# Kernel optimization log

Hardware: AMD Instinct MI355X
Metric: run time of the kernel (lower is better)

Reference implementation:

```python
import jax, jax.numpy as jnp
import numpy as np
from jax import lax

B, T, V, C = 16, 128, 137, 3
IOC = [(64, 64), (64, 128), (128, 256)]  # (in_c, out_c), all strides 1
OUT0 = 64
K = 9
PAD = (K - 1) // 2
NUM_CLASS = 226
DELTA = 0.5
BN_EPS = 1e-5


def setup_inputs() -> dict:
    key = jax.random.key(0)
    ks = jax.random.split(key, 16)
    inp = {"X": jax.random.normal(ks[0], (B, T, V, C), dtype=jnp.float32)}
    # data_bn params over V*C channels
    inp["bn_gamma"] = jnp.ones((V * C,), jnp.float32)
    inp["bn_beta"] = jnp.zeros((V * C,), jnp.float32)
    # gtcn0 conv
    inp["w0"] = jax.random.normal(ks[1], (OUT0, C, K, 1), jnp.float32) * np.sqrt(2.0 / (C * K))
    inp["b0"] = jnp.zeros((OUT0,), jnp.float32)
    for i, (ic, oc) in enumerate(IOC):
        inp[f"w{i+1}"] = jax.random.normal(ks[2 + i], (oc, ic, K, 1), jnp.float32) * np.sqrt(2.0 / (ic * K))
        inp[f"b{i+1}"] = jnp.zeros((oc,), jnp.float32)
    inp["fc_w"] = jax.random.normal(ks[8], (NUM_CLASS, IOC[-1][1]), jnp.float32) * 0.02
    inp["fc_b"] = jnp.zeros((NUM_CLASS,), jnp.float32)
    return inp


def _adj(X):
    # Gaussian-kernel affinity per (batch, frame): exp(-||xi-xj|| / (2*delta^2)).
    # Original builds this on CPU with scipy.cdist inside torch.tensor (detached),
    # so we stop gradients through it.
    Xs = lax.stop_gradient(X)  # [B,T,V,C]
    diff = Xs[:, :, :, None, :] - Xs[:, :, None, :, :]  # [B,T,V,V,C]
    dist = jnp.sqrt(jnp.sum(diff * diff, axis=-1))       # euclidean, like cdist
    return jnp.exp(-dist / (2.0 * DELTA ** 2))            # [B,T,V,V]


def _conv(x, w, b):
    # Conv2d kernel (K,1), padding ((K-1)//2, 0), stride (1,1)
    y = lax.conv_general_dilated(x, w, window_strides=(1, 1),
                                 padding=[(PAD, PAD), (0, 0)],
                                 dimension_numbers=("NCHW", "OIHW", "NCHW"))
    return y + b[None, :, None, None]


def reference(X, bn_gamma, bn_beta, w0, b0, w1, b1, w2, b2, w3, b3, fc_w, fc_b):
    A = _adj(X)  # [B,T,V,V]
    # data_bn: BatchNorm1d over V*C channels (training-mode batch stats)
    Xr = jnp.einsum("btvc->bvct", X).reshape(B, V * C, T)
    mean = Xr.mean(axis=(0, 2), keepdims=True)
    var = Xr.var(axis=(0, 2), keepdims=True)
    Xn = (Xr - mean) * jax.lax.rsqrt(var + BN_EPS)
    Xn = Xn * bn_gamma[None, :, None] + bn_beta[None, :, None]
    x = jnp.einsum("bvct->bctv", Xn.reshape(B, V, C, T))  # [B,C,T,V]
    x = _conv(x, w0, b0)
    for w, b in ((w1, b1), (w2, b2), (w3, b3)):
        ax = jnp.einsum("bctv,btvw->bctw", x, A)  # graph matmul X @ A per (b,t)
        x = jax.nn.relu(_conv(ax, w, b))
    x = x.mean(axis=(2, 3))  # [B, C_out]
    return x @ fc_w.T + fc_b  # [B, num_class]
```

## Files before the change

kernel.cpp:

```cpp
#include <hip/hip_runtime.h>
#include <hip/hip_bf16.h>
#include <math.h>

#define BB 16
#define TT 128
#define VV 137
#define CCH 3
#define NN (VV*TT)
#define NCLS 226
#define APITCH 23040

typedef __attribute__((ext_vector_type(8))) short bf16x8;
typedef __attribute__((ext_vector_type(4))) float f32x4;

__device__ __forceinline__ unsigned short f2bf(float x) {
  __hip_bfloat16 h = __float2bfloat16(x);
  return *reinterpret_cast<unsigned short*>(&h);
}

__device__ __forceinline__ void gld_lds16(const unsigned short* src, unsigned short* ldst) {
  __builtin_amdgcn_global_load_lds(
      (const __attribute__((address_space(1))) void*)src,
      (__attribute__((address_space(3))) void*)ldst, 16, 0, 0);
}

__global__ void bn_stats_kernel(const float* __restrict__ X,
                                const float* __restrict__ gamma,
                                const float* __restrict__ beta,
                                float* __restrict__ scale,
                                float* __restrict__ shift) {
  const int ch = blockIdx.x;
  const int v = ch / CCH, c = ch % CCH;
  const int tid = threadIdx.x;
  float s = 0.f, q = 0.f;
  for (int idx = tid; idx < BB*TT; idx += 256) {
    float x = X[(idx*VV + v)*CCH + c];
    s += x; q += x*x;
  }
  #pragma unroll
  for (int off = 32; off > 0; off >>= 1) {
    s += __shfl_down(s, off, 64);
    q += __shfl_down(q, off, 64);
  }
  __shared__ float ls[4], lq[4];
  const int wid = tid >> 6, lane = tid & 63;
  if (lane == 0) { ls[wid] = s; lq[wid] = q; }
  __syncthreads();
  if (tid == 0) {
    float S = ls[0]+ls[1]+ls[2]+ls[3];
    float Q = lq[0]+lq[1]+lq[2]+lq[3];
    const float inv_n = 1.f / (BB*TT);
    float mean = S * inv_n;
    float var = Q * inv_n - mean*mean;
    float sc = gamma[ch] * rsqrtf(var + 1e-5f);
    scale[ch] = sc;
    shift[ch] = beta[ch] - mean * sc;
  }
}

__global__ void bn_apply_v(const float* __restrict__ X,
                           const float* __restrict__ scale,
                           const float* __restrict__ shift,
                           unsigned short* __restrict__ xn) {
  const int o = blockIdx.x*256 + threadIdx.x;
  if (o >= BB*NN*CCH) return;
  const int c = o % CCH;
  const int n = (o / CCH) % NN;
  const int b = o / (CCH*NN);
  const int v = n >> 7, t = n & 127;
  const int ch = v*CCH + c;
  float val = X[((b*TT + t)*VV + v)*CCH + c] * scale[ch] + shift[ch];
  xn[o] = f2bf(val);
}

__global__ void wtrans_kernel(const float* __restrict__ w, unsigned short* __restrict__ wT,
                              int OC, int IC) {
  const int o = blockIdx.x*256 + threadIdx.x;
  if (o >= OC*IC*9) return;
  const int ic = o % IC;
  const int oc = (o / IC) % OC;
  const int kk = o / (IC*OC);
  wT[o] = f2bf(w[(oc*IC + ic)*9 + kk]);
}

__global__ void w0trans_kernel(const float* __restrict__ w0, unsigned short* __restrict__ w0T) {
  const int o = blockIdx.x*256 + threadIdx.x;
  if (o >= 64*32) return;
  const int k = o % 32, oc = o / 32;
  const int kk = k / 3, ic = k % 3;
  w0T[o] = (k < 27) ? f2bf(w0[(oc*3 + ic)*9 + kk]) : (unsigned short)0;
}

__global__ void zero_kernel(float* __restrict__ p, int n) {
  const int i = blockIdx.x*256 + threadIdx.x;
  if (i < n) p[i] = 0.f;
}

__global__ __launch_bounds__(256)
void adj_v(const float* __restrict__ X, unsigned short* __restrict__ A) {
  __shared__ float Xs[3][144];
  const int b = blockIdx.x / TT, t = blockIdx.x % TT;
  const int tid = threadIdx.x;
  for (int i = tid; i < 3*VV; i += 256) {
    const int c = i / VV, v = i % VV;
    Xs[c][v] = X[((b*TT + t)*VV + v)*CCH + c];
  }
  __syncthreads();
  unsigned short* Ab = A + (size_t)blockIdx.x * APITCH;
  for (int e = tid; e < 144*160; e += 256) {
    const int w = e / 160, v = e % 160;
    unsigned short val = 0;
    if (w < VV && v < VV) {
      const float d0 = Xs[0][v]-Xs[0][w];
      const float d1 = Xs[1][v]-Xs[1][w];
      const float d2 = Xs[2][v]-Xs[2][w];
      val = f2bf(__expf(-2.f * sqrtf(d0*d0 + d1*d1 + d2*d2)));
    }
    Ab[e] = val;
  }
}

__global__ __launch_bounds__(256)
void conv0_v(const unsigned short* __restrict__ xn,
             const unsigned short* __restrict__ w0T,
             const float* __restrict__ bias,
             unsigned short* __restrict__ outp) {
  __shared__ unsigned short im_s[128*40];
  __shared__ unsigned short w_s[64*40];
  __shared__ unsigned short ob[128*72];
  const int tid = threadIdx.x;
  const int v0 = blockIdx.x % 137;
  const int b  = blockIdx.x / 137;
  const int wave = tid >> 6, lane = tid & 63, quad = lane >> 4, l15 = lane & 15;
  const int mh = wave * 32;

  {
    const int row = tid >> 2, cg = tid & 3;
    *(uint4*)&w_s[row*40 + cg*8] = *(const uint4*)(w0T + row*32 + cg*8);
  }
  for (int e = tid; e < 128*32; e += 256) {
    const int t = e >> 5, k = e & 31;
    unsigned short val = 0;
    if (k < 27) {
      const int kk = k / 3, ic = k % 3;
      const int tp = t + kk - 4;
      if (tp >= 0 && tp < TT)
        val = xn[((size_t)b*NN + (size_t)v0*TT + tp)*3 + ic];
    }
    im_s[t*40 + k] = val;
  }
  __syncthreads();

  f32x4 acc[2][4];
  #pragma unroll
  for (int mt = 0; mt < 2; ++mt)
    #pragma unroll
    for (int ct = 0; ct < 4; ++ct) acc[mt][ct] = (f32x4){0.f,0.f,0.f,0.f};

  bf16x8 af[2], bfr[4];
  #pragma unroll
  for (int mt = 0; mt < 2; ++mt)
    af[mt] = *(const bf16x8*)&im_s[(mh + mt*16 + l15)*40 + quad*8];
  #pragma unroll
  for (int ct = 0; ct < 4; ++ct)
    bfr[ct] = *(const bf16x8*)&w_s[(ct*16 + l15)*40 + quad*8];
  #pragma unroll
  for (int mt = 0; mt < 2; ++mt)
    #pragma unroll
    for (int ct = 0; ct < 4; ++ct)
      acc[mt][ct] = __builtin_amdgcn_mfma_f32_16x16x32_bf16(af[mt], bfr[ct], acc[mt][ct], 0, 0, 0);

  #pragma unroll
  for (int mt = 0; mt < 2; ++mt) {
    const int tb = mh + mt*16 + quad*4;
    #pragma unroll
    for (int ct = 0; ct < 4; ++ct) {
      const int oc = ct*16 + l15;
      const float bv = bias[oc];
      #pragma unroll
      for (int r = 0; r < 4; ++r)
        ob[(tb + r)*72 + oc] = f2bf(acc[mt][ct][r] + bv);
    }
  }
  __syncthreads();
  for (int rr = 0; rr < 4; ++rr) {
    const int idx = rr*256 + tid;
    const int t = idx >> 3, cg = idx & 7;
    uint4 val = *(const uint4*)&ob[t*72 + cg*8];
    *(uint4*)(outp + ((size_t)b*NN + (size_t)v0*TT + t)*64 + cg*8) = val;
  }
}

template<int IC, int OCB, int VROWS, int WDBUF, int RELU, int FUSE>
__global__ __launch_bounds__(256)
void conv_v3(const unsigned short* __restrict__ in,
             const unsigned short* __restrict__ wT,
             const float* __restrict__ bias,
             unsigned short* __restrict__ outp,
             float* __restrict__ mout,
             const unsigned short* __restrict__ zbuf,
             int OCtot, int nocb) {
  constexpr int NCT  = (VROWS == 2) ? OCB/16 : OCB/32;
  constexpr int NWIN = 136*IC/512;
  constexpr int TWIN = VROWS*NWIN;
  constexpr int WWIN = OCB*IC/512;
  constexpr int GPR  = IC/8;
  constexpr int RPW  = 512/IC;
  constexpr int INSZ = VROWS*136*IC;
  constexpr int WSZ  = OCB*IC;
  constexpr int NWB  = WDBUF ? 2 : 1;
  constexpr int OCP  = OCB + 8;
  constexpr int OBSZ = FUSE ? 0 : VROWS*128*OCP;
  constexpr int TOT  = (INSZ + NWB*WSZ > OBSZ) ? (INSZ + NWB*WSZ) : OBSZ;
  __shared__ unsigned short sh[TOT];
  unsigned short* in_s = sh;
  unsigned short* ob = sh;

  const int tid = threadIdx.x;
  const int wave = tid >> 6, lane = tid & 63, quad = lane >> 4, l15 = lane & 15;
  const int nv = (VROWS == 2) ? 69 : 137;
  const int grp  = blockIdx.x % nv;
  const int ocby = (blockIdx.x / nv) % nocb;
  const int b    = blockIdx.x / (nv*nocb);
  const int v0 = grp * VROWS;
  const int ocb0 = ocby * OCB;
  const int vr  = (VROWS == 2) ? (wave >> 1) : 0;
  const int mhl = (VROWS == 2) ? ((wave & 1) * 64) : ((wave >> 1) * 64);
  const int chb = (VROWS == 2) ? 0 : ((wave & 1) * (OCB >> 1));
  const bool vok = (VROWS == 1) || ((v0 + vr) < VV);

  const int lrow = lane / GPR;
  const int lg   = lane % GPR;

  #pragma unroll
  for (int wi = 0; wi < (TWIN+3)/4; ++wi) {
    const int W = wave + 4*wi;
    if (W < TWIN) {
      const int vrW = W / NWIN;
      const int rl = (W % NWIN)*RPW + lrow;
      const int t = rl - 4;
      const int sg = lg ^ (rl & 7);
      const unsigned short* src = (t >= 0 && t < TT && (v0+vrW) < VV)
          ? in + ((size_t)b*NN + (size_t)(v0+vrW)*TT + t)*IC + (sg<<3)
          : zbuf + lane*8;
      gld_lds16(src, in_s + W*512);
    }
  }
  auto stage_w = [&](int kk, int buf) {
    unsigned short* wb = sh + INSZ + buf*WSZ;
    #pragma unroll
    for (int wi = 0; wi < WWIN/4; ++wi) {
      const int W = wave + 4*wi;
      const int row = W*RPW + lrow;
      const int sg = lg ^ (row & 7);
      gld_lds16(wT + ((size_t)kk*OCtot + ocb0 + row)*IC + (sg<<3), wb + W*512);
    }
  };

  f32x4 acc[4][NCT];
  #pragma unroll
  for (int mt = 0; mt < 4; ++mt)
    #pragma unroll
    for (int ct = 0; ct < NCT; ++ct) acc[mt][ct] = (f32x4){0.f,0.f,0.f,0.f};

  auto compute_kk = [&](int kk, int buf) {
    const unsigned short* wb = sh + INSZ + buf*WSZ;
    #pragma unroll
    for (int ks = 0; ks < IC/32; ++ks) {
      const int G = ks*4 + quad;
      bf16x8 af[4], bfr[NCT];
      #pragma unroll
      for (int mt = 0; mt < 4; ++mt) {
        const int row = mhl + mt*16 + l15 + kk;
        af[mt] = *(const bf16x8*)&in_s[vr*(136*IC) + row*IC + ((G ^ (row & 7)) << 3)];
      }
      #pragma unroll
      for (int ct = 0; ct < NCT; ++ct) {
        const int row = chb + ct*16 + l15;
        bfr[ct] = *(const bf16x8*)&wb[row*IC + ((G ^ (row & 7)) << 3)];
      }
      #pragma unroll
      for (int mt = 0; mt < 4; ++mt)
        #pragma unroll
        for (int ct = 0; ct < NCT; ++ct)
          acc[mt][ct] = __builtin_amdgcn_mfma_f32_16x16x32_bf16(af[mt], bfr[ct], acc[mt][ct], 0, 0, 0);
    }
  };

  if (WDBUF) {
    stage_w(0, 0);
    __syncthreads();
    for (int kk = 0; kk < 9; ++kk) {
      if (kk < 8) stage_w(kk+1, (kk+1) & 1);
      compute_kk(kk, kk & 1);
      __syncthreads();
    }
  } else {
    for (int kk = 0; kk < 9; ++kk) {
      stage_w(kk, 0);
      __syncthreads();
      compute_kk(kk, 0);
      __syncthreads();
    }
  }

  if (FUSE) {
    if (vok) {
      #pragma unroll
      for (int ct = 0; ct < NCT; ++ct) {
        const int oc = ocb0 + chb + ct*16 + l15;
        const float bv = bias[oc];
        float s = 0.f;
        #pragma unroll
        for (int mt = 0; mt < 4; ++mt)
          #pragma unroll
          for (int r = 0; r < 4; ++r) {
            float x = acc[mt][ct][r] + bv;
            if (RELU) x = fmaxf(x, 0.f);
            s += x;
          }
        s += __shfl_down(s, 32, 64);
        s += __shfl_down(s, 16, 64);
        if (lane < 16) atomicAdd(&mout[(size_t)b*OCtot + oc], s * (1.f / NN));
      }
    }
  } else {
    #pragma unroll
    for (int mt = 0; mt < 4; ++mt) {
      const int ro = vr*128 + mhl + mt*16 + quad*4;
      #pragma unroll
      for (int ct = 0; ct < NCT; ++ct) {
        const int oc = chb + ct*16 + l15;
        const float bv = bias[ocb0 + oc];
        #pragma unroll
        for (int r = 0; r < 4; ++r) {
          float x = acc[mt][ct][r] + bv;
          if (RELU) x = fmaxf(x, 0.f);
          ob[(ro + r)*OCP + oc] = f2bf(x);
        }
      }
    }
    __syncthreads();
    constexpr int GPO = OCB/8;
    #pragma unroll
    for (int it = 0; it < VROWS*128*GPO/256; ++it) {
      const int task = it*256 + tid;
      const int ro = task / GPO, g = task % GPO;
      const int vrow = v0 + (ro >> 7);
      if (vrow < VV) {
        uint4 val = *(const uint4*)&ob[ro*OCP + g*8];
        *(uint4*)(outp + ((size_t)b*NN + (size_t)vrow*TT + (ro & 127))*OCB + g*8) = val;
      }
    }
  }
}

__global__ __launch_bounds__(256)
void gmm_v3(const unsigned short* __restrict__ A,
            const unsigned short* __restrict__ act,
            unsigned short* __restrict__ outp,
            int Cfull) {
  __shared__ unsigned short sh[12288 + APITCH];
  unsigned short* xt = sh;
  unsigned short* As = sh + 12288;
  unsigned short* ob = sh + 12288;
  const int bt = blockIdx.x;
  const int b = bt / TT, t = bt % TT;
  const int ch = blockIdx.y;
  const int tid = threadIdx.x;
  const int wave = tid >> 6, lane = tid & 63, quad = lane >> 4, l15 = lane & 15;

  const unsigned short* Abt = A + (size_t)bt * APITCH;
  for (int W = wave; W < 45; W += 4)
    gld_lds16(Abt + W*512 + lane*8, As + W*512);

  #pragma unroll
  for (int it = 0; it < 5; ++it) {
    const int task = it*256 + tid;
    const int v = task >> 3, g = task & 7;
    uint4 val = {0u,0u,0u,0u};
    if (v < VV)
      val = *(const uint4*)(act + ((size_t)b*NN + (size_t)v*TT + t)*Cfull + ch*64 + g*8);
    const unsigned short* pv = (const unsigned short*)&val;
    const int vg = v >> 3, vrm = v & 7;
    #pragma unroll
    for (int j = 0; j < 8; ++j) {
      const int c = g*8 + j;
      const int slot = ((vg ^ (c & 7) ^ ((c >> 3) & 7)) << 3) | vrm;
      xt[c*192 + slot] = pv[j];
    }
  }
  __syncthreads();

  f32x4 acc[9];
  #pragma unroll
  for (int ct = 0; ct < 9; ++ct) acc[ct] = (f32x4){0.f,0.f,0.f,0.f};

  const int m = wave*16 + l15;
  #pragma unroll
  for (int ks = 0; ks < 5; ++ks) {
    const int G = ks*4 + quad;
    const int slot = (G ^ (m & 7) ^ ((m >> 3) & 7)) << 3;
    const bf16x8 af = *(const bf16x8*)&xt[m*192 + slot];
    #pragma unroll
    for (int ct = 0; ct < 9; ++ct) {
      const bf16x8 bfv = *(const bf16x8*)&As[(ct*16 + l15)*160 + ks*32 + quad*8];
      acc[ct] = __builtin_amdgcn_mfma_f32_16x16x32_bf16(af, bfv, acc[ct], 0, 0, 0);
    }
  }
  __syncthreads();

  #pragma unroll
  for (int ct = 0; ct < 9; ++ct) {
    const int w = ct*16 + l15;
    #pragma unroll
    for (int r = 0; r < 4; ++r) {
      const int c = wave*16 + quad*4 + r;
      ob[w*72 + c] = f2bf(acc[ct][r]);
    }
  }
  __syncthreads();
  {
    const int wl = tid >> 3, cg = tid & 7;
    #pragma unroll
    for (int rr = 0; rr < 5; ++rr) {
      const int w = rr*32 + wl;
      if (w < VV) {
        uint4 val = *(const uint4*)&ob[w*72 + cg*8];
        *(uint4*)(outp + ((size_t)b*NN + (size_t)w*TT + t)*Cfull + ch*64 + cg*8) = val;
      }
    }
  }
}

__global__ void fc_kernel(const float* __restrict__ mean,
                          const float* __restrict__ fcw,
                          const float* __restrict__ fcb,
                          float* __restrict__ out) {
  const int b = blockIdx.x;
  __shared__ float ms[256];
  const int tid = threadIdx.x;
  ms[tid] = mean[b*256 + tid];
  __syncthreads();
  if (tid < NCLS) {
    float acc = fcb[tid];
    for (int c = 0; c < 256; ++c) acc = fmaf(ms[c], fcw[tid*256 + c], acc);
    out[b*NCLS + tid] = acc;
  }
}

extern "C" void kernel_launch(void* const* d_in, const int* in_sizes, int n_in,
                              void* d_out, int out_size, void* d_ws, size_t ws_size,
                              hipStream_t stream) {
  const float* X    = (const float*)d_in[0];
  const float* bn_g = (const float*)d_in[1];
  const float* bn_b = (const float*)d_in[2];
  const float* w0   = (const float*)d_in[3];
  const float* cb0  = (const float*)d_in[4];
  const float* w1   = (const float*)d_in[5];
  const float* cb1  = (const float*)d_in[6];
  const float* w2   = (const float*)d_in[7];
  const float* cb2  = (const float*)d_in[8];
  const float* w3   = (const float*)d_in[9];
  const float* cb3  = (const float*)d_in[10];
  const float* fcw  = (const float*)d_in[11];
  const float* fcb  = (const float*)d_in[12];
  float* out = (float*)d_out;

  unsigned char* W = (unsigned char*)d_ws;
  size_t off = 0;
  auto alloc = [&](size_t bytes) -> void* {
    void* p = W + off;
    off += (bytes + 255) & ~(size_t)255;
    return p;
  };
  float* meanb  = (float*)alloc(BB*256*4);
  float* zbuf_f = (float*)alloc(2048);
  float* scale  = (float*)alloc(512*4);
  float* shiftb = (float*)alloc(512*4);
  unsigned short* w0T = (unsigned short*)alloc(64*32*2);
  unsigned short* wT1 = (unsigned short*)alloc((size_t)9*64*64*2);
  unsigned short* wT2 = (unsigned short*)alloc((size_t)9*128*64*2);
  unsigned short* wT3 = (unsigned short*)alloc((size_t)9*256*128*2);
  unsigned short* xn  = (unsigned short*)alloc((size_t)BB*NN*3*2);
  const size_t fixedB = off;
  const size_t perB = 2*((size_t)NN*128*2 + 256) + ((size_t)TT*APITCH*2 + 256);

  int g = 1;
  if (ws_size > fixedB + perB) {
    size_t gg = (ws_size - fixedB) / perB;
    g = (gg >= BB) ? BB : (int)gg;
  }
  unsigned short* P  = (unsigned short*)alloc((size_t)g*NN*128*2);
  unsigned short* Q  = (unsigned short*)alloc((size_t)g*NN*128*2);
  unsigned short* Ab = (unsigned short*)alloc((size_t)g*TT*APITCH*2);
  const unsigned short* zbuf = (const unsigned short*)zbuf_f;

  bn_stats_kernel<<<411, 256, 0, stream>>>(X, bn_g, bn_b, scale, shiftb);
  bn_apply_v<<<(BB*NN*3 + 255)/256, 256, 0, stream>>>(X, scale, shiftb, xn);
  w0trans_kernel<<<(64*32 + 255)/256, 256, 0, stream>>>(w0, w0T);
  wtrans_kernel<<<(9*64*64   + 255)/256, 256, 0, stream>>>(w1, wT1, 64, 64);
  wtrans_kernel<<<(9*128*64  + 255)/256, 256, 0, stream>>>(w2, wT2, 128, 64);
  wtrans_kernel<<<(9*256*128 + 255)/256, 256, 0, stream>>>(w3, wT3, 256, 128);
  zero_kernel<<<((BB*256 + 512) + 255)/256, 256, 0, stream>>>(meanb, BB*256 + 512);

  for (int b0 = 0; b0 < BB; b0 += g) {
    const int gb = (BB - b0 < g) ? (BB - b0) : g;
    const float* Xg = X + (size_t)b0 * TT * VV * CCH;
    const unsigned short* xng = xn + (size_t)b0 * NN * 3;
    float* mg = meanb + (size_t)b0 * 256;

    adj_v<<<gb*TT, 256, 0, stream>>>(Xg, Ab);
    conv0_v<<<137*gb, 256, 0, stream>>>(xng, w0T, cb0, P);
    gmm_v3<<<dim3(gb*TT, 1), 256, 0, stream>>>(Ab, P, Q, 64);
    conv_v3<64,64,1,1,1,0><<<137*gb, 256, 0, stream>>>(Q, wT1, cb1, P, nullptr, zbuf, 64, 1);
    gmm_v3<<<dim3(gb*TT, 1), 256, 0, stream>>>(Ab, P, Q, 64);
    conv_v3<64,128,1,1,1,0><<<137*gb, 256, 0, stream>>>(Q, wT2, cb2, P, nullptr, zbuf, 128, 1);
    gmm_v3<<<dim3(gb*TT, 2), 256, 0, stream>>>(Ab, P, Q, 128);
    conv_v3<128,128,1,0,1,1><<<137*2*gb, 256, 0, stream>>>(Q, wT3, cb3, nullptr, mg, zbuf, 256, 2);
  }

  fc_kernel<<<BB, 256, 0, stream>>>(meanb, fcw, fcb, out);
}
```

Before: 528.4 us.

## Load conv weights directly into registers with double-buffered prefetch, drop LDS weight staging

The temporal conv kernel no longer stages weight tiles in LDS with per-tap barriers. Each lane loads its MFMA B-fragments straight from global memory (L2-resident) into registers, ping-ponging two register buffers across k-steps, and the unused VROWS=2 path is removed. This cuts LDS size and the barriers inside the main loop, which may improve occupancy and overlap. In exchange every wave re-reads the weights from global or L2 and uses more registers, and load latency is only hidden by a one-step prefetch.

Measured after the change: 735.6 us. 39.2% more time.

```diff
diff --git a/kernel.cpp b/kernel.cpp
--- a/kernel.cpp
+++ b/kernel.cpp
@@ -191,70 +191,62 @@
   }
 }
 
-template<int IC, int OCB, int VROWS, int WDBUF, int RELU, int FUSE>
+template<int IC, int OCB, int RELU, int FUSE>
 __global__ __launch_bounds__(256)
-void conv_v3(const unsigned short* __restrict__ in,
+void conv_v4(const unsigned short* __restrict__ in,
              const unsigned short* __restrict__ wT,
              const float* __restrict__ bias,
              unsigned short* __restrict__ outp,
              float* __restrict__ mout,
              const unsigned short* __restrict__ zbuf,
              int OCtot, int nocb) {
-  constexpr int NCT  = (VROWS == 2) ? OCB/16 : OCB/32;
+  constexpr int NCT  = OCB/32;
+  constexpr int KS   = IC/32;
+  constexpr int NSTEP= 9*KS;
   constexpr int NWIN = 136*IC/512;
-  constexpr int TWIN = VROWS*NWIN;
-  constexpr int WWIN = OCB*IC/512;
   constexpr int GPR  = IC/8;
   constexpr int RPW  = 512/IC;
-  constexpr int INSZ = VROWS*136*IC;
-  constexpr int WSZ  = OCB*IC;
-  constexpr int NWB  = WDBUF ? 2 : 1;
+  constexpr int INSZ = 136*IC;
   constexpr int OCP  = OCB + 8;
-  constexpr int OBSZ = FUSE ? 0 : VROWS*128*OCP;
-  constexpr int TOT  = (INSZ + NWB*WSZ > OBSZ) ? (INSZ + NWB*WSZ) : OBSZ;
+  constexpr int OBSZ = FUSE ? 0 : 128*OCP;
+  constexpr int TOT  = (INSZ > OBSZ) ? INSZ : OBSZ;
   __shared__ unsigned short sh[TOT];
   unsigned short* in_s = sh;
   unsigned short* ob = sh;
 
   const int tid = threadIdx.x;
   const int wave = tid >> 6, lane = tid & 63, quad = lane >> 4, l15 = lane & 15;
-  const int nv = (VROWS == 2) ? 69 : 137;
-  const int grp  = blockIdx.x % nv;
-  const int ocby = (blockIdx.x / nv) % nocb;
-  const int b    = blockIdx.x / (nv*nocb);
-  const int v0 = grp * VROWS;
+  const int v0   = blockIdx.x % 137;
+  const int ocby = (blockIdx.x / 137) % nocb;
+  const int b    = blockIdx.x / (137*nocb);
   const int ocb0 = ocby * OCB;
-  const int vr  = (VROWS == 2) ? (wave >> 1) : 0;
-  const int mhl = (VROWS == 2) ? ((wave & 1) * 64) : ((wave >> 1) * 64);
-  const int chb = (VROWS == 2) ? 0 : ((wave & 1) * (OCB >> 1));
-  const bool vok = (VROWS == 1) || ((v0 + vr) < VV);
+  const int mhl = (wave >> 1) * 64;
+  const int chb = (wave & 1) * (OCB >> 1);
 
   const int lrow = lane / GPR;
   const int lg   = lane % GPR;
 
   #pragma unroll
-  for (int wi = 0; wi < (TWIN+3)/4; ++wi) {
+  for (int wi = 0; wi < (NWIN+3)/4; ++wi) {
     const int W = wave + 4*wi;
-    if (W < TWIN) {
-      const int vrW = W / NWIN;
-      const int rl = (W % NWIN)*RPW + lrow;
+    if (W < NWIN) {
+      const int rl = W*RPW + lrow;
       const int t = rl - 4;
       const int sg = lg ^ (rl & 7);
-      const unsigned short* src = (t >= 0 && t < TT && (v0+vrW) < VV)
-          ? in + ((size_t)b*NN + (size_t)(v0+vrW)*TT + t)*IC + (sg<<3)
+      const unsigned short* src = (t >= 0 && t < TT)
+          ? in + ((size_t)b*NN + (size_t)v0*TT + t)*IC + (sg<<3)
           : zbuf + lane*8;
       gld_lds16(src, in_s + W*512);
     }
   }
-  auto stage_w = [&](int kk, int buf) {
-    unsigned short* wb = sh + INSZ + buf*WSZ;
-    #pragma unroll
-    for (int wi = 0; wi < WWIN/4; ++wi) {
-      const int W = wave + 4*wi;
-      const int row = W*RPW + lrow;
-      const int sg = lg ^ (row & 7);
-      gld_lds16(wT + ((size_t)kk*OCtot + ocb0 + row)*IC + (sg<<3), wb + W*512);
-    }
+
+  const unsigned short* wbase = wT + ((size_t)(ocb0 + chb + l15))*IC + quad*8;
+  auto wload = [&](int s, bf16x8 (&wr)[NCT]) {
+    const int kk = s / KS, ks = s - kk*KS;
+    const unsigned short* p = wbase + ((size_t)kk*OCtot)*IC + ks*32;
+    #pragma unroll
+    for (int ct = 0; ct < NCT; ++ct)
+      wr[ct] = *(const bf16x8*)(p + ct*16*IC);
   };
 
   f32x4 acc[4][NCT];
@@ -263,71 +255,57 @@
     #pragma unroll
     for (int ct = 0; ct < NCT; ++ct) acc[mt][ct] = (f32x4){0.f,0.f,0.f,0.f};
 
-  auto compute_kk = [&](int kk, int buf) {
-    const unsigned short* wb = sh + INSZ + buf*WSZ;
-    #pragma unroll
-    for (int ks = 0; ks < IC/32; ++ks) {
-      const int G = ks*4 + quad;
-      bf16x8 af[4], bfr[NCT];
+  auto compute_step = [&](int kk, int ks, bf16x8 (&wr)[NCT]) {
+    const int G = ks*4 + quad;
+    bf16x8 af[4];
+    #pragma unroll
+    for (int mt = 0; mt < 4; ++mt) {
+      const int row = mhl + mt*16 + l15 + kk;
+      af[mt] = *(const bf16x8*)&in_s[row*IC + ((G ^ (row & 7)) << 3)];
+    }
+    #pragma unroll
+    for (int mt = 0; mt < 4; ++mt)
       #pragma unroll
-      for (int mt = 0; mt < 4; ++mt) {
-        const int row = mhl + mt*16 + l15 + kk;
-        af[mt] = *(const bf16x8*)&in_s[vr*(136*IC) + row*IC + ((G ^ (row & 7)) << 3)];
-      }
-      #pragma unroll
-      for (int ct = 0; ct < NCT; ++ct) {
-        const int row = chb + ct*16 + l15;
-        bfr[ct] = *(const bf16x8*)&wb[row*IC + ((G ^ (row & 7)) << 3)];
-      }
+      for (int ct = 0; ct < NCT; ++ct)
+        acc[mt][ct] = __builtin_amdgcn_mfma_f32_16x16x32_bf16(af[mt], wr[ct], acc[mt][ct], 0, 0, 0);
+  };
+
+  bf16x8 wA[NCT], wB[NCT];
+  wload(0, wA);
+  wload(1, wB);
+  __syncthreads();
+
+  #pragma unroll
+  for (int s = 0; s < NSTEP; s += 2) {
+    compute_step(s / KS, s % KS, wA);
+    if (s + 2 < NSTEP) wload(s + 2, wA);
+    compute_step((s+1) / KS, (s+1) % KS, wB);
+    if (s + 3 < NSTEP) wload(s + 3, wB);
+  }
+
+  if (FUSE) {
+    #pragma unroll
+    for (int ct = 0; ct < NCT; ++ct) {
+      const int oc = ocb0 + chb + ct*16 + l15;
+      const float bv = bias[oc];
+      float s = 0.f;
       #pragma unroll
       for (int mt = 0; mt < 4; ++mt)
         #pragma unroll
-        for (int ct = 0; ct < NCT; ++ct)
-          acc[mt][ct] = __builtin_amdgcn_mfma_f32_16x16x32_bf16(af[mt], bfr[ct], acc[mt][ct], 0, 0, 0);
-    }
-  };
-
-  if (WDBUF) {
-    stage_w(0, 0);
+        for (int r = 0; r < 4; ++r) {
+          float x = acc[mt][ct][r] + bv;
+          if (RELU) x = fmaxf(x, 0.f);
+          s += x;
+        }
+      s += __shfl_down(s, 32, 64);
+      s += __shfl_down(s, 16, 64);
+      if (lane < 16) atomicAdd(&mout[(size_t)b*OCtot + oc], s * (1.f / NN));
+    }
+  } else {
     __syncthreads();
-    for (int kk = 0; kk < 9; ++kk) {
-      if (kk < 8) stage_w(kk+1, (kk+1) & 1);
-      compute_kk(kk, kk & 1);
-      __syncthreads();
-    }
-  } else {
-    for (int kk = 0; kk < 9; ++kk) {
-      stage_w(kk, 0);
-      __syncthreads();
-      compute_kk(kk, 0);
-      __syncthreads();
-    }
-  }
-
-  if (FUSE) {
-    if (vok) {
-      #pragma unroll
-      for (int ct = 0; ct < NCT; ++ct) {
-        const int oc = ocb0 + chb + ct*16 + l15;
-        const float bv = bias[oc];
-        float s = 0.f;
-        #pragma unroll
-        for (int mt = 0; mt < 4; ++mt)
-          #pragma unroll
-          for (int r = 0; r < 4; ++r) {
-            float x = acc[mt][ct][r] + bv;
-            if (RELU) x = fmaxf(x, 0.f);
-            s += x;
-          }
-        s += __shfl_down(s, 32, 64);
-        s += __shfl_down(s, 16, 64);
-        if (lane < 16) atomicAdd(&mout[(size_t)b*OCtot + oc], s * (1.f / NN));
-      }
-    }
-  } else {
     #pragma unroll
     for (int mt = 0; mt < 4; ++mt) {
-      const int ro = vr*128 + mhl + mt*16 + quad*4;
+      const int ro = mhl + mt*16 + quad*4;
       #pragma unroll
       for (int ct = 0; ct < NCT; ++ct) {
         const int oc = chb + ct*16 + l15;
@@ -343,14 +321,11 @@
     __syncthreads();
     constexpr int GPO = OCB/8;
     #pragma unroll
-    for (int it = 0; it < VROWS*128*GPO/256; ++it) {
+    for (int it = 0; it < 128*GPO/256; ++it) {
       const int task = it*256 + tid;
       const int ro = task / GPO, g = task % GPO;
-      const int vrow = v0 + (ro >> 7);
-      if (vrow < VV) {
-        uint4 val = *(const uint4*)&ob[ro*OCP + g*8];
-        *(uint4*)(outp + ((size_t)b*NN + (size_t)vrow*TT + (ro & 127))*OCB + g*8) = val;
-      }
+      uint4 val = *(const uint4*)&ob[ro*OCP + g*8];
+      *(uint4*)(outp + ((size_t)b*NN + (size_t)v0*TT + ro)*OCB + g*8) = val;
     }
   }
 }
@@ -513,11 +488,11 @@
     adj_v<<<gb*TT, 256, 0, stream>>>(Xg, Ab);
     conv0_v<<<137*gb, 256, 0, stream>>>(xng, w0T, cb0, P);
     gmm_v3<<<dim3(gb*TT, 1), 256, 0, stream>>>(Ab, P, Q, 64);
-    conv_v3<64,64,1,1,1,0><<<137*gb, 256, 0, stream>>>(Q, wT1, cb1, P, nullptr, zbuf, 64, 1);
+    conv_v4<64,64,1,0><<<137*gb, 256, 0, stream>>>(Q, wT1, cb1, P, nullptr, zbuf, 64, 1);
     gmm_v3<<<dim3(gb*TT, 1), 256, 0, stream>>>(Ab, P, Q, 64);
-    conv_v3<64,128,1,1,1,0><<<137*gb, 256, 0, stream>>>(Q, wT2, cb2, P, nullptr, zbuf, 128, 1);
+    conv_v4<64,128,1,0><<<137*gb, 256, 0, stream>>>(Q, wT2, cb2, P, nullptr, zbuf, 128, 1);
     gmm_v3<<<dim3(gb*TT, 2), 256, 0, stream>>>(Ab, P, Q, 128);
-    conv_v3<128,128,1,0,1,1><<<137*2*gb, 256, 0, stream>>>(Q, wT3, cb3, nullptr, mg, zbuf, 256, 2);
+    conv_v4<128,128,1,1><<<137*2*gb, 256, 0, stream>>>(Q, wT3, cb3, nullptr, mg, zbuf, 256, 2);
   }
 
   fc_kernel<<<BB, 256, 0, stream>>>(meanb, fcw, fcb, out);
```

## Merge prep kernels into one launch and fuse BN apply into conv0

Applied to the files above, without the earlier changes.

Merges BN statistics, the first batch-group adjacency build, weight transposes and buffer zeroing into a single heterogeneous mega_prep kernel dispatched by block index. The separate BN-apply pass is removed: conv0 now reads raw X and applies scale/shift while building its im2col tile. This cuts several launches and one intermediate write/read of the normalized input. The cost is strided fp32 loads of X inside conv0 and a mixed-role prep kernel whose blocks have uneven work.

New measurement: 544.5 us. +3.0%, slower.

```diff
diff --git a/kernel.cpp b/kernel.cpp
--- a/kernel.cpp
+++ b/kernel.cpp
@@ -24,12 +24,12 @@
       (__attribute__((address_space(3))) void*)ldst, 16, 0, 0);
 }
 
-__global__ void bn_stats_kernel(const float* __restrict__ X,
-                                const float* __restrict__ gamma,
-                                const float* __restrict__ beta,
-                                float* __restrict__ scale,
-                                float* __restrict__ shift) {
-  const int ch = blockIdx.x;
+__device__ void bn_stats_body(const float* __restrict__ X,
+                              const float* __restrict__ gamma,
+                              const float* __restrict__ beta,
+                              float* __restrict__ scale,
+                              float* __restrict__ shift,
+                              int ch, float* sm) {
   const int v = ch / CCH, c = ch % CCH;
   const int tid = threadIdx.x;
   float s = 0.f, q = 0.f;
@@ -42,13 +42,12 @@
     s += __shfl_down(s, off, 64);
     q += __shfl_down(q, off, 64);
   }
-  __shared__ float ls[4], lq[4];
   const int wid = tid >> 6, lane = tid & 63;
-  if (lane == 0) { ls[wid] = s; lq[wid] = q; }
+  if (lane == 0) { sm[wid] = s; sm[4 + wid] = q; }
   __syncthreads();
   if (tid == 0) {
-    float S = ls[0]+ls[1]+ls[2]+ls[3];
-    float Q = lq[0]+lq[1]+lq[2]+lq[3];
+    float S = sm[0]+sm[1]+sm[2]+sm[3];
+    float Q = sm[4]+sm[5]+sm[6]+sm[7];
     const float inv_n = 1.f / (BB*TT);
     float mean = S * inv_n;
     float var = Q * inv_n - mean*mean;
@@ -58,62 +57,23 @@
   }
 }
 
-__global__ void bn_apply_v(const float* __restrict__ X,
-                           const float* __restrict__ scale,
-                           const float* __restrict__ shift,
-                           unsigned short* __restrict__ xn) {
-  const int o = blockIdx.x*256 + threadIdx.x;
-  if (o >= BB*NN*CCH) return;
-  const int c = o % CCH;
-  const int n = (o / CCH) % NN;
-  const int b = o / (CCH*NN);
-  const int v = n >> 7, t = n & 127;
-  const int ch = v*CCH + c;
-  float val = X[((b*TT + t)*VV + v)*CCH + c] * scale[ch] + shift[ch];
-  xn[o] = f2bf(val);
-}
-
-__global__ void wtrans_kernel(const float* __restrict__ w, unsigned short* __restrict__ wT,
-                              int OC, int IC) {
-  const int o = blockIdx.x*256 + threadIdx.x;
-  if (o >= OC*IC*9) return;
-  const int ic = o % IC;
-  const int oc = (o / IC) % OC;
-  const int kk = o / (IC*OC);
-  wT[o] = f2bf(w[(oc*IC + ic)*9 + kk]);
-}
-
-__global__ void w0trans_kernel(const float* __restrict__ w0, unsigned short* __restrict__ w0T) {
-  const int o = blockIdx.x*256 + threadIdx.x;
-  if (o >= 64*32) return;
-  const int k = o % 32, oc = o / 32;
-  const int kk = k / 3, ic = k % 3;
-  w0T[o] = (k < 27) ? f2bf(w0[(oc*3 + ic)*9 + kk]) : (unsigned short)0;
-}
-
-__global__ void zero_kernel(float* __restrict__ p, int n) {
-  const int i = blockIdx.x*256 + threadIdx.x;
-  if (i < n) p[i] = 0.f;
-}
-
-__global__ __launch_bounds__(256)
-void adj_v(const float* __restrict__ X, unsigned short* __restrict__ A) {
-  __shared__ float Xs[3][144];
-  const int b = blockIdx.x / TT, t = blockIdx.x % TT;
+__device__ void adj_body(const float* __restrict__ X, unsigned short* __restrict__ A,
+                         int bt, float* XsF) {
+  const int b = bt / TT, t = bt % TT;
   const int tid = threadIdx.x;
   for (int i = tid; i < 3*VV; i += 256) {
     const int c = i / VV, v = i % VV;
-    Xs[c][v] = X[((b*TT + t)*VV + v)*CCH + c];
-  }
-  __syncthreads();
-  unsigned short* Ab = A + (size_t)blockIdx.x * APITCH;
+    XsF[c*144 + v] = X[((b*TT + t)*VV + v)*CCH + c];
+  }
+  __syncthreads();
+  unsigned short* Ab = A + (size_t)bt * APITCH;
   for (int e = tid; e < 144*160; e += 256) {
     const int w = e / 160, v = e % 160;
     unsigned short val = 0;
     if (w < VV && v < VV) {
-      const float d0 = Xs[0][v]-Xs[0][w];
-      const float d1 = Xs[1][v]-Xs[1][w];
-      const float d2 = Xs[2][v]-Xs[2][w];
+      const float d0 = XsF[v]       - XsF[w];
+      const float d1 = XsF[144 + v] - XsF[144 + w];
+      const float d2 = XsF[288 + v] - XsF[288 + w];
       val = f2bf(__expf(-2.f * sqrtf(d0*d0 + d1*d1 + d2*d2)));
     }
     Ab[e] = val;
@@ -121,7 +81,58 @@
 }
 
 __global__ __launch_bounds__(256)
-void conv0_v(const unsigned short* __restrict__ xn,
+void mega_prep(const float* __restrict__ X,
+               const float* __restrict__ bn_g, const float* __restrict__ bn_b,
+               const float* __restrict__ w0, const float* __restrict__ w1,
+               const float* __restrict__ w2, const float* __restrict__ w3,
+               float* __restrict__ scale, float* __restrict__ shift,
+               float* __restrict__ zmem,
+               unsigned short* __restrict__ w0T, unsigned short* __restrict__ wT1,
+               unsigned short* __restrict__ wT2, unsigned short* __restrict__ wT3,
+               unsigned short* __restrict__ A, int nadj) {
+  __shared__ float sm[3*144];
+  int blk = blockIdx.x;
+  if (blk < 411) { bn_stats_body(X, bn_g, bn_b, scale, shift, blk, sm); return; }
+  blk -= 411;
+  if (blk < nadj) { adj_body(X, A, blk, sm); return; }
+  blk -= nadj;
+  const int i = blk*256 + threadIdx.x;
+  const int NZ = BB*256 + 512;
+  if (i < NZ) { zmem[i] = 0.f; return; }
+  int o = i - NZ;
+  if (o < 64*32) {
+    const int k = o & 31, oc = o >> 5;
+    const int kk = k / 3, ic = k % 3;
+    w0T[o] = (k < 27) ? f2bf(w0[(oc*3 + ic)*9 + kk]) : (unsigned short)0;
+    return;
+  }
+  o -= 64*32;
+  if (o < 9*64*64) {
+    const int ic = o & 63, oc = (o >> 6) & 63, kk = o >> 12;
+    wT1[o] = f2bf(w1[(oc*64 + ic)*9 + kk]); return;
+  }
+  o -= 9*64*64;
+  if (o < 9*128*64) {
+    const int ic = o & 63, oc = (o >> 6) & 127, kk = o >> 13;
+    wT2[o] = f2bf(w2[(oc*64 + ic)*9 + kk]); return;
+  }
+  o -= 9*128*64;
+  if (o < 9*256*128) {
+    const int ic = o & 127, oc = (o >> 7) & 255, kk = o >> 15;
+    wT3[o] = f2bf(w3[(oc*128 + ic)*9 + kk]); return;
+  }
+}
+
+__global__ __launch_bounds__(256)
+void adj_v(const float* __restrict__ X, unsigned short* __restrict__ A) {
+  __shared__ float XsF[3*144];
+  adj_body(X, A, blockIdx.x, XsF);
+}
+
+__global__ __launch_bounds__(256)
+void conv0_v(const float* __restrict__ X,
+             const float* __restrict__ scale,
+             const float* __restrict__ shift,
              const unsigned short* __restrict__ w0T,
              const float* __restrict__ bias,
              unsigned short* __restrict__ outp) {
@@ -144,8 +155,10 @@
     if (k < 27) {
       const int kk = k / 3, ic = k % 3;
       const int tp = t + kk - 4;
-      if (tp >= 0 && tp < TT)
-        val = xn[((size_t)b*NN + (size_t)v0*TT + tp)*3 + ic];
+      if (tp >= 0 && tp < TT) {
+        const float x = X[((size_t)(b*TT + tp)*VV + v0)*3 + ic];
+        val = f2bf(x * scale[v0*3 + ic] + shift[v0*3 + ic]);
+      }
     }
     im_s[t*40 + k] = val;
   }
@@ -482,7 +495,6 @@
   unsigned short* wT1 = (unsigned short*)alloc((size_t)9*64*64*2);
   unsigned short* wT2 = (unsigned short*)alloc((size_t)9*128*64*2);
   unsigned short* wT3 = (unsigned short*)alloc((size_t)9*256*128*2);
-  unsigned short* xn  = (unsigned short*)alloc((size_t)BB*NN*3*2);
   const size_t fixedB = off;
   const size_t perB = 2*((size_t)NN*128*2 + 256) + ((size_t)TT*APITCH*2 + 256);
 
@@ -496,22 +508,19 @@
   unsigned short* Ab = (unsigned short*)alloc((size_t)g*TT*APITCH*2);
   const unsigned short* zbuf = (const unsigned short*)zbuf_f;
 
-  bn_stats_kernel<<<411, 256, 0, stream>>>(X, bn_g, bn_b, scale, shiftb);
-  bn_apply_v<<<(BB*NN*3 + 255)/256, 256, 0, stream>>>(X, scale, shiftb, xn);
-  w0trans_kernel<<<(64*32 + 255)/256, 256, 0, stream>>>(w0, w0T);
-  wtrans_kernel<<<(9*64*64   + 255)/256, 256, 0, stream>>>(w1, wT1, 64, 64);
-  wtrans_kernel<<<(9*128*64  + 255)/256, 256, 0, stream>>>(w2, wT2, 128, 64);
-  wtrans_kernel<<<(9*256*128 + 255)/256, 256, 0, stream>>>(w3, wT3, 256, 128);
-  zero_kernel<<<((BB*256 + 512) + 255)/256, 256, 0, stream>>>(meanb, BB*256 + 512);
+  const int gb0 = (g < BB) ? g : BB;
+  const int nadj = gb0 * TT;
+  mega_prep<<<411 + nadj + 1610, 256, 0, stream>>>(
+      X, bn_g, bn_b, w0, w1, w2, w3, scale, shiftb, meanb,
+      w0T, wT1, wT2, wT3, Ab, nadj);
 
   for (int b0 = 0; b0 < BB; b0 += g) {
     const int gb = (BB - b0 < g) ? (BB - b0) : g;
     const float* Xg = X + (size_t)b0 * TT * VV * CCH;
-    const unsigned short* xng = xn + (size_t)b0 * NN * 3;
     float* mg = meanb + (size_t)b0 * 256;
 
-    adj_v<<<gb*TT, 256, 0, stream>>>(Xg, Ab);
-    conv0_v<<<137*gb, 256, 0, stream>>>(xng, w0T, cb0, P);
+    if (b0 > 0) adj_v<<<gb*TT, 256, 0, stream>>>(Xg, Ab);
+    conv0_v<<<137*gb, 256, 0, stream>>>(Xg, scale, shiftb, w0T, cb0, P);
     gmm_v3<<<dim3(gb*TT, 1), 256, 0, stream>>>(Ab, P, Q, 64);
     conv_v3<64,64,1,1,1,0><<<137*gb, 256, 0, stream>>>(Q, wT1, cb1, P, nullptr, zbuf, 64, 1);
     gmm_v3<<<dim3(gb*TT, 1), 256, 0, stream>>>(Ab, P, Q, 64);
```
